# Optimization experiments

Hardware: AMD Instinct MI355X
Metric: run time of the kernel (lower is better)

The kernel has to match this reference:

```python
import jax, jax.numpy as jnp
import numpy as np

LOG2PI = float(np.log(2.0 * np.pi))
NUM_GROUPS = 32
WEIGHTS_THRESHOLD = 0.01
ACTIVATION_THRESHOLD = 1e-9


def _cdist(a, b):
    # a: (..., N, 3), b: (..., M, 3) -> (..., N, M) euclidean distances
    d2 = (jnp.sum(a * a, -1)[..., :, None]
          + jnp.sum(b * b, -1)[..., None, :]
          - 2.0 * jnp.einsum('...nd,...md->...nm', a, b))
    return jnp.sqrt(jnp.maximum(d2, 0.0))


def setup_inputs() -> dict:
    key = jax.random.key(0)
    ks = jax.random.split(key, 7)
    B, V, O, G = 16, 778, 8192, NUM_GROUPS
    verts = jax.random.normal(ks[0], (B, V, 3), jnp.float32)
    anchor_verts = jax.random.normal(ks[1], (B, G, 3), jnp.float32)
    obj_pts = jax.random.normal(ks[2], (B, O, 3), jnp.float32)
    raw = jax.random.normal(ks[3], (B, G, 12), jnp.float32)
    mean = raw[..., :3]
    M = raw[..., 3:].reshape(B, G, 3, 3)
    cov = jnp.einsum('bgij,bgkj->bgik', M, M) + 1e-2 * jnp.eye(3, dtype=jnp.float32)
    contact_gaussians = jnp.concatenate([mean, cov.reshape(B, G, 9)], axis=-1)
    obj_normals = jax.random.normal(ks[4], (B, O, 6), jnp.float32)
    init_verts = jax.random.normal(ks[5], (V, 3), jnp.float32)
    init_anchors = jax.random.normal(ks[6], (G, 3), jnp.float32)
    return dict(verts=verts, anchor_verts=anchor_verts, obj_pts=obj_pts,
                contact_gaussians=contact_gaussians, obj_normals=obj_normals,
                init_verts=init_verts, init_anchors=init_anchors, K=5)


def reference(verts, anchor_verts, obj_pts, contact_gaussians, obj_normals,
              init_verts, init_anchors, K):
    B, V, _ = verts.shape
    G = NUM_GROUPS
    # __init__: assign each vertex to its closest anchor (partition into 32 groups)
    gid = jnp.argmin(_cdist(init_verts, init_anchors), axis=-1)  # (V,)

    # KNN: K smallest distances vertex -> object points
    neigh = _cdist(verts, obj_pts)                 # (B, V, O)
    knn = -jax.lax.top_k(-neigh, K)[0]             # (B, V, K)

    # Per-group MVN log-prob for every vertex (G=32 small, V=778 small)
    mean = contact_gaussians[:, :, :3] + anchor_verts          # (B, G, 3)
    cov = contact_gaussians[:, :, 3:].reshape(B, G, 3, 3)
    L = jnp.linalg.cholesky(cov)                               # (B, G, 3, 3)
    diff = verts[:, None, :, :] - mean[:, :, None, :]          # (B, G, V, 3)
    y = jax.scipy.linalg.solve_triangular(L[:, :, None], diff[..., None], lower=True)[..., 0]
    maha = jnp.sum(y * y, -1)                                  # (B, G, V)
    half_logdet = jnp.sum(jnp.log(jnp.diagonal(L, axis1=-2, axis2=-1)), -1)  # (B, G)
    logp = -0.5 * (maha + 3.0 * LOG2PI) - half_logdet[:, :, None]
    w_all = jnp.exp(logp)                                      # (B, G, V)
    # pick each vertex's own group's weight
    idx = jnp.broadcast_to(gid[None, None, :], (B, 1, V))
    w = jnp.take_along_axis(w_all, idx, axis=1)[:, 0]          # (B, V)

    # per-group min/max normalization (masked, groups partition the vertices)
    grp_mask = gid[None, :] == jnp.arange(G)[:, None]          # (G, V)
    seg_min = jnp.min(jnp.where(grp_mask[None], w[:, None, :], jnp.inf), -1)   # (B, G)
    seg_max = jnp.max(jnp.where(grp_mask[None], w[:, None, :], -jnp.inf), -1)  # (B, G)
    mn = seg_min[:, gid]
    mx = seg_max[:, gid]
    wn = (w - mn) / (mx - mn)
    wn = jnp.where(wn > WEIGHTS_THRESHOLD, wn, 0.0)

    # group activation: torch.allclose(cg[:, i], 0) over whole batch -> zero weight
    active = jnp.any(jnp.abs(contact_gaussians) > ACTIVATION_THRESHOLD, axis=(0, 2))  # (G,)
    eff = jnp.where(active[gid][None, :], wn, 0.0)             # (B, V)
    distances = knn * eff[..., None]
    d_mean = jnp.mean(distances)

    # penetration regularizer using nearest object normal
    ovd = _cdist(verts, obj_normals[..., :3])                  # (B, V, O)
    nn_idx = jnp.argmin(ovd, -1)                               # (B, V)
    nn = jnp.take_along_axis(obj_normals, nn_idx[..., None], axis=1)  # (B, V, 6)
    roots = nn[..., :3] - 0.002 * nn[..., 3:]
    dp = jnp.einsum('bvi,bvi->bv', nn[..., 3:], verts - roots)
    pen = jnp.mean(jax.nn.relu(-dp))
    return (d_mean, pen)
```

## Files before the change

kernel.cpp:

```cpp
#include <hip/hip_runtime.h>
#include <math.h>

#define BB 16
#define VV 778
#define OO 8192
#define GG 32
#define KNN 5
#define VHALF 389
#define THREE_LOG2PI 5.513631199228036f

#define MED3 __builtin_amdgcn_fmed3f

__device__ __forceinline__ void insert5_med3(float (&t)[KNN], float s) {
    t[4] = MED3(s, t[3], t[4]);
    t[3] = MED3(s, t[2], t[3]);
    t[2] = MED3(s, t[1], t[2]);
    t[1] = MED3(s, t[0], t[1]);
    t[0] = fminf(t[0], s);
}

__device__ __forceinline__ void merge5_med3(float (&m)[KNN], const float (&b)[KNN]) {
    m[4] = MED3(b[0], m[3], m[4]);
    m[3] = MED3(b[0], m[2], m[3]);
    m[2] = MED3(b[0], m[1], m[2]);
    m[1] = MED3(b[0], m[0], m[1]);
    m[0] = fminf(m[0], b[0]);
    m[4] = MED3(b[1], m[3], m[4]);
    m[3] = MED3(b[1], m[2], m[3]);
    m[2] = MED3(b[1], m[1], m[2]);
    m[1] = fminf(m[1], b[1]);
    m[4] = MED3(b[2], m[3], m[4]);
    m[3] = MED3(b[2], m[2], m[3]);
    m[2] = fminf(m[2], b[2]);
    m[4] = MED3(b[3], m[3], m[4]);
    m[3] = fminf(m[3], b[3]);
    m[4] = fminf(m[4], b[4]);
}

template <int LOGP1, int LOGP2>
__global__ __launch_bounds__(256) void scan_kernel(
    const float* __restrict__ verts,
    const float* __restrict__ anchor_verts,
    const float* __restrict__ obj_pts,
    const float* __restrict__ contact_gaussians,
    const float* __restrict__ obj_normals,
    const float* __restrict__ init_verts,
    const float* __restrict__ init_anchors,
    int* __restrict__ gid_ws,
    float* __restrict__ active_ws,
    float* __restrict__ segmn,
    float* __restrict__ segmx,
    float* __restrict__ w_ws,
    float* __restrict__ top5,
    float* __restrict__ nns,
    int* __restrict__ nni,
    float* __restrict__ out) {
    constexpr int P1 = 1 << LOGP1;
    constexpr int NPTS1 = OO >> LOGP1;
    constexpr int CH1 = (NPTS1 < 512) ? NPTS1 : 512;
    constexpr int P2 = 1 << LOGP2;
    constexpr int NPTS2 = OO >> LOGP2;
    constexpr int CH2 = (NPTS2 < 512) ? NPTS2 : 512;
    constexpr int CHMAX = (CH1 > CH2) ? CH1 : CH2;

    __shared__ float4 tile[CHMAX];
    __shared__ float anc[GG * 4];
    __shared__ float cholb[GG * 10];
    __shared__ unsigned short gidl[VV];
    __shared__ unsigned int smn[GG], smx[GG];

    int tid = threadIdx.x;
    int bid = blockIdx.x;

    if (bid < BB * 2 * P1) {
        int vc = bid & 1;
        int p = (bid >> 1) & (P1 - 1);
        int b = bid >> (1 + LOGP1);

        int v0 = vc * VHALF + tid;
        bool val1 = (256 + tid) < VHALF;
        int v1 = v0 + (val1 ? 256 : 0);

        float X0, Y0, Z0, X1, Y1, Z1;
        {
            const float* vp = verts + ((size_t)b * VV + v0) * 3;
            X0 = -2.0f * vp[0]; Y0 = -2.0f * vp[1]; Z0 = -2.0f * vp[2];
            const float* vq = verts + ((size_t)b * VV + v1) * 3;
            X1 = -2.0f * vq[0]; Y1 = -2.0f * vq[1]; Z1 = -2.0f * vq[2];
        }

        float t0[KNN], t1[KNN];
#pragma unroll
        for (int k = 0; k < KNN; ++k) { t0[k] = INFINITY; t1[k] = INFINITY; }

        const float* pb = obj_pts + ((size_t)b * OO + p * NPTS1) * 3;
        for (int c0 = 0; c0 < NPTS1; c0 += CH1) {
            for (int j = tid; j < CH1; j += 256) {
                const float* q = pb + (size_t)(c0 + j) * 3;
                float a0 = q[0], a1 = q[1], a2 = q[2];
                tile[j] = make_float4(a0, a1, a2, a0 * a0 + a1 * a1 + a2 * a2);
            }
            __syncthreads();
#pragma unroll 8
            for (int i = 0; i < CH1; ++i) {
                float4 q = tile[i];
                float s0 = fmaf(X0, q.x, fmaf(Y0, q.y, fmaf(Z0, q.z, q.w)));
                float s1 = fmaf(X1, q.x, fmaf(Y1, q.y, fmaf(Z1, q.z, q.w)));
                insert5_med3(t0, s0);
                insert5_med3(t1, s1);
            }
            __syncthreads();
        }
        {
            size_t base = ((size_t)(b * P1 + p) * KNN) * VV;
#pragma unroll
            for (int k = 0; k < KNN; ++k) top5[base + (size_t)k * VV + v0] = t0[k];
            if (val1) {
#pragma unroll
                for (int k = 0; k < KNN; ++k) top5[base + (size_t)k * VV + v1] = t1[k];
            }
        }
        return;
    }

    {
        int sub = bid - BB * 2 * P1;
        int vc = sub & 1;
        int p = (sub >> 1) & (P2 - 1);
        int b = sub >> (1 + LOGP2);

        bool wduty = (p == 0 && vc == 0);
        bool aduty = (p == 0 && vc == 1 && b == 0);
        if (wduty || aduty) {
            if (tid < GG) {
                float x = init_anchors[tid * 3 + 0];
                float y = init_anchors[tid * 3 + 1];
                float z = init_anchors[tid * 3 + 2];
                anc[tid * 4 + 0] = x; anc[tid * 4 + 1] = y;
                anc[tid * 4 + 2] = z; anc[tid * 4 + 3] = x * x + y * y + z * z;
                smn[tid] = 0x7F800000u;
                smx[tid] = 0u;
                if (wduty) {
                    const float* cg2 = contact_gaussians + ((size_t)b * GG + tid) * 12;
                    const float* av = anchor_verts + ((size_t)b * GG + tid) * 3;
                    float c00 = cg2[3];
                    float c10 = cg2[6], c11 = cg2[7];
                    float c20 = cg2[9], c21 = cg2[10], c22 = cg2[11];
                    float L00 = sqrtf(c00);
                    float L10 = c10 / L00;
                    float L20 = c20 / L00;
                    float L11 = sqrtf(c11 - L10 * L10);
                    float L21 = (c21 - L20 * L10) / L11;
                    float L22 = sqrtf(c22 - L20 * L20 - L21 * L21);
                    float* c = cholb + tid * 10;
                    c[0] = L00; c[1] = L10; c[2] = L11;
                    c[3] = L20; c[4] = L21; c[5] = L22;
                    c[6] = logf(L00) + logf(L11) + logf(L22);
                    c[7] = cg2[0] + av[0];
                    c[8] = cg2[1] + av[1];
                    c[9] = cg2[2] + av[2];
                }
            }
            __syncthreads();
            for (int v = tid; v < VV; v += 256) {
                float x = init_verts[v * 3 + 0];
                float y = init_verts[v * 3 + 1];
                float z = init_verts[v * 3 + 2];
                float vv = x * x + y * y + z * z;
                float best = INFINITY;
                int bg = 0;
                for (int g = 0; g < GG; ++g) {
                    float d2 = vv + anc[g * 4 + 3] -
                               2.0f * (x * anc[g * 4 + 0] + y * anc[g * 4 + 1] + z * anc[g * 4 + 2]);
                    d2 = fmaxf(d2, 0.0f);
                    if (d2 < best) { best = d2; bg = g; }
                }
                gidl[v] = (unsigned short)bg;
                if (aduty) gid_ws[v] = bg;
            }
            __syncthreads();
            if (wduty) {
                for (int v = tid; v < VV; v += 256) {
                    int g = gidl[v];
                    const float* c = cholb + g * 10;
                    const float* vp = verts + ((size_t)b * VV + v) * 3;
                    float d0 = vp[0] - c[7];
                    float d1 = vp[1] - c[8];
                    float d2 = vp[2] - c[9];
                    float y0 = d0 / c[0];
                    float y1 = (d1 - c[1] * y0) / c[2];
                    float y2 = (d2 - c[3] * y0 - c[4] * y1) / c[5];
                    float maha = y0 * y0 + y1 * y1 + y2 * y2;
                    float wv = expf(-0.5f * (maha + THREE_LOG2PI) - c[6]);
                    w_ws[(size_t)b * VV + v] = wv;
                    unsigned int u = __float_as_uint(wv);
                    atomicMin(&smn[g], u);
                    atomicMax(&smx[g], u);
                }
                __syncthreads();
                if (tid < GG) {
                    segmn[b * GG + tid] = __uint_as_float(smn[tid]);
                    segmx[b * GG + tid] = __uint_as_float(smx[tid]);
                }
            }
            if (aduty) {
                if (tid < GG) {
                    int any = 0;
                    for (int bb = 0; bb < BB && !any; ++bb) {
                        for (int c = 0; c < 12; ++c) {
                            if (fabsf(contact_gaussians[((size_t)bb * GG + tid) * 12 + c]) > 1e-9f) {
                                any = 1;
                                break;
                            }
                        }
                    }
                    active_ws[tid] = any ? 1.0f : 0.0f;
                }
                if (tid == 0) { out[0] = 0.0f; out[1] = 0.0f; }
            }
            __syncthreads();
        }

        int v0 = vc * VHALF + tid;
        bool val1 = (256 + tid) < VHALF;
        int v1 = v0 + (val1 ? 256 : 0);

        float X0, Y0, Z0, X1, Y1, Z1;
        {
            const float* vp = verts + ((size_t)b * VV + v0) * 3;
            X0 = -2.0f * vp[0]; Y0 = -2.0f * vp[1]; Z0 = -2.0f * vp[2];
            const float* vq = verts + ((size_t)b * VV + v1) * 3;
            X1 = -2.0f * vq[0]; Y1 = -2.0f * vq[1]; Z1 = -2.0f * vq[2];
        }

        float bs0 = INFINITY, bs1 = INFINITY;
        int bi0 = 0, bi1 = 0;
        const float* nbp = obj_normals + ((size_t)b * OO + p * NPTS2) * 6;
        for (int c0 = 0; c0 < NPTS2; c0 += CH2) {
            for (int j = tid; j < CH2; j += 256) {
                const float* r = nbp + (size_t)(c0 + j) * 6;
                float b0 = r[0], b1 = r[1], b2 = r[2];
                tile[j] = make_float4(b0, b1, b2, b0 * b0 + b1 * b1 + b2 * b2);
            }
            __syncthreads();
#pragma unroll 8
            for (int i = 0; i < CH2; ++i) {
                float4 n = tile[i];
                float u0 = fmaf(X0, n.x, fmaf(Y0, n.y, fmaf(Z0, n.z, n.w)));
                float u1 = fmaf(X1, n.x, fmaf(Y1, n.y, fmaf(Z1, n.z, n.w)));
                int gi = c0 + i;
                if (u0 < bs0) { bs0 = u0; bi0 = gi; }
                if (u1 < bs1) { bs1 = u1; bi1 = gi; }
            }
            __syncthreads();
        }
        {
            size_t o = (size_t)(b * P2 + p) * VV + v0;
            nns[o] = bs0;
            nni[o] = p * NPTS2 + bi0;
            if (val1) {
                size_t o1 = (size_t)(b * P2 + p) * VV + v1;
                nns[o1] = bs1;
                nni[o1] = p * NPTS2 + bi1;
            }
        }
    }
}

template <int LOGP1, int LOGP2>
__global__ __launch_bounds__(256) void finalize_kernel(
    const float* __restrict__ top5,
    const float* __restrict__ nns,
    const int* __restrict__ nni,
    const float* __restrict__ obj_normals,
    const float* __restrict__ verts,
    const int* __restrict__ gid,
    const float* __restrict__ w,
    const float* __restrict__ segmn,
    const float* __restrict__ segmx,
    const float* __restrict__ active,
    float* __restrict__ out) {
    constexpr int P1 = 1 << LOGP1;
    constexpr int P2 = 1 << LOGP2;
    constexpr int NM1 = (P1 + 3) / 4;
    constexpr int NM2 = (P2 + 3) / 4;
    constexpr int NCH = (VV + 63) / 64;

    __shared__ float mt[4][KNN][64];
    __shared__ float sb[4][64];
    __shared__ int ib[4][64];
    __shared__ float rd[256], rp[256];

    int tid = threadIdx.x;
    int pi = tid >> 6;
    int vi = tid & 63;
    int b = blockIdx.x / NCH;
    int chunk = blockIdx.x - b * NCH;
    int v = chunk * 64 + vi;
    bool valid = v < VV;

    float m[KNN];
#pragma unroll
    for (int k = 0; k < KNN; ++k) m[k] = INFINITY;
    if (valid) {
#pragma unroll
        for (int r = 0; r < NM1; ++r) {
            int p = pi * NM1 + r;
            if (p < P1) {
                size_t base = ((size_t)(b * P1 + p) * KNN) * VV + v;
                float t[KNN];
#pragma unroll
                for (int k = 0; k < KNN; ++k) t[k] = top5[base + (size_t)k * VV];
                merge5_med3(m, t);
            }
        }
    }

    float bs = INFINITY;
    int bi = 0x7FFFFFFF;
    if (valid) {
#pragma unroll
        for (int r = 0; r < NM2; ++r) {
            int p = pi * NM2 + r;
            if (p < P2) {
                size_t o = (size_t)(b * P2 + p) * VV + v;
                float s = nns[o];
                int i = nni[o];
                if (s < bs || (s == bs && i < bi)) { bs = s; bi = i; }
            }
        }
    }

#pragma unroll
    for (int k = 0; k < KNN; ++k) mt[pi][k][vi] = m[k];
    sb[pi][vi] = bs;
    ib[pi][vi] = bi;
    __syncthreads();

    if (pi < 2) {
        float t[KNN];
#pragma unroll
        for (int k = 0; k < KNN; ++k) t[k] = mt[pi + 2][k][vi];
        merge5_med3(m, t);
#pragma unroll
        for (int k = 0; k < KNN; ++k) mt[pi][k][vi] = m[k];
        float s = sb[pi + 2][vi];
        int i = ib[pi + 2][vi];
        if (s < bs || (s == bs && i < bi)) { bs = s; bi = i; }
        sb[pi][vi] = bs;
        ib[pi][vi] = bi;
    }
    __syncthreads();

    float cd = 0.0f, cp = 0.0f;
    if (pi == 0 && valid) {
        float t[KNN];
#pragma unroll
        for (int k = 0; k < KNN; ++k) t[k] = mt[1][k][vi];
        merge5_med3(m, t);
        float s = sb[1][vi];
        int i = ib[1][vi];
        if (s < bs || (s == bs && i < bi)) { bs = s; bi = i; }

        const float* vp = verts + ((size_t)b * VV + v) * 3;
        float vx = vp[0], vy = vp[1], vz = vp[2];
        float vv = vx * vx + vy * vy + vz * vz;

        int g = gid[v];
        float wv = w[(size_t)b * VV + v];
        float mn = segmn[b * GG + g];
        float mx = segmx[b * GG + g];
        float wn = (wv - mn) / (mx - mn);
        float eff = (active[g] != 0.0f && wn > 0.01f) ? wn : 0.0f;
        float sk = 0.0f;
#pragma unroll
        for (int k = 0; k < KNN; ++k) sk += sqrtf(fmaxf(vv + m[k], 0.0f));
        cd = eff * sk;

        const float* row = obj_normals + ((size_t)b * OO + bi) * 6;
        float n0 = row[3], n1 = row[4], n2 = row[5];
        float r0 = row[0] - 0.002f * n0;
        float r1 = row[1] - 0.002f * n1;
        float r2 = row[2] - 0.002f * n2;
        float dp = n0 * (vx - r0) + n1 * (vy - r1) + n2 * (vz - r2);
        cp = fmaxf(-dp, 0.0f);
    }

    rd[tid] = cd;
    rp[tid] = cp;
    __syncthreads();
    for (int s = 128; s > 0; s >>= 1) {
        if (tid < s) {
            rd[tid] += rd[tid + s];
            rp[tid] += rp[tid + s];
        }
        __syncthreads();
    }
    if (tid == 0) {
        atomicAdd(&out[0], rd[0] * (1.0f / ((float)BB * VV * KNN)));
        atomicAdd(&out[1], rp[0] * (1.0f / ((float)BB * VV)));
    }
}

template <int LOGP1, int LOGP2>
static void launch_all(const float* verts, const float* anchor_verts,
                       const float* obj_pts, const float* contact_gaussians,
                       const float* obj_normals, const float* init_verts,
                       const float* init_anchors, int* gid_ws, float* active_ws,
                       float* segmn, float* segmx, float* w_ws, float* top5,
                       float* nns, int* nni, float* out, hipStream_t stream) {
    constexpr int P1 = 1 << LOGP1;
    constexpr int P2 = 1 << LOGP2;
    constexpr int NCH = (VV + 63) / 64;
    dim3 block(256);
    hipLaunchKernelGGL((scan_kernel<LOGP1, LOGP2>), dim3(BB * 2 * (P1 + P2)), block,
                       0, stream, verts, anchor_verts, obj_pts, contact_gaussians,
                       obj_normals, init_verts, init_anchors, gid_ws, active_ws,
                       segmn, segmx, w_ws, top5, nns, nni, out);
    hipLaunchKernelGGL((finalize_kernel<LOGP1, LOGP2>), dim3(BB * NCH),
                       block, 0, stream, top5, nns, nni, obj_normals, verts,
                       gid_ws, w_ws, segmn, segmx, active_ws, out);
}

extern "C" void kernel_launch(void* const* d_in, const int* in_sizes, int n_in,
                              void* d_out, int out_size, void* d_ws, size_t ws_size,
                              hipStream_t stream) {
    const float* verts = (const float*)d_in[0];
    const float* anchor_verts = (const float*)d_in[1];
    const float* obj_pts = (const float*)d_in[2];
    const float* contact_gaussians = (const float*)d_in[3];
    const float* obj_normals = (const float*)d_in[4];
    const float* init_verts = (const float*)d_in[5];
    const float* init_anchors = (const float*)d_in[6];
    float* out = (float*)d_out;

    char* ws = (char*)d_ws;
    int* gid_ws = (int*)(ws + 0);
    float* active_ws = (float*)(ws + 4096);
    float* segmn = (float*)(ws + 4224);
    float* segmx = (float*)(ws + 6272);
    float* w_ws = (float*)(ws + 8320);
    const size_t base = 58112;

    int logP1 = 5;
    while (logP1 > 0) {
        int P1 = 1 << logP1, P2 = 1 << (logP1 > 0 ? logP1 - 1 : 0);
        if (base + (size_t)BB * VV * 4 * (P1 * KNN + P2 * 2) <= ws_size) break;
        --logP1;
    }
    int P1 = 1 << logP1;
    int logP2 = logP1 > 0 ? logP1 - 1 : 0;
    int P2 = 1 << logP2;

    float* top5 = (float*)(ws + base);
    float* nns = (float*)(ws + base + (size_t)BB * P1 * KNN * VV * 4);
    int* nni = (int*)(ws + base + (size_t)BB * VV * 4 * (P1 * KNN + P2));

#define LAUNCH(L1, L2)                                                         \
    launch_all<L1, L2>(verts, anchor_verts, obj_pts, contact_gaussians,        \
                       obj_normals, init_verts, init_anchors, gid_ws,          \
                       active_ws, segmn, segmx, w_ws, top5, nns, nni, out,     \
                       stream)
    switch (logP1) {
        case 5: LAUNCH(5, 4); break;
        case 4: LAUNCH(4, 3); break;
        case 3: LAUNCH(3, 2); break;
        case 2: LAUNCH(2, 1); break;
        case 1: LAUNCH(1, 0); break;
        default: LAUNCH(0, 0); break;
    }
#undef LAUNCH
}
```

Baseline: 144.1 us.

## Process all vertices per block and reduce nearest-normal index with 64-bit atomicMin

Each scan block now covers all 778 vertices (four per thread) instead of splitting them across two blocks, so every loaded object tile is reused across twice as many vertices. The nearest-normal partial results are no longer written to workspace and merged in finalize. Instead each block packs an order-preserving distance key and the point index into a 64-bit value and applies atomicMin, which needs a memset before launch. The nearest-normal search gets as many partitions as the KNN scan. The price is higher register pressure, fewer and larger blocks, and an extra memset launch.

```diff
diff --git a/kernel.cpp b/kernel.cpp
--- a/kernel.cpp
+++ b/kernel.cpp
@@ -6,7 +6,6 @@
 #define OO 8192
 #define GG 32
 #define KNN 5
-#define VHALF 389
 #define THREE_LOG2PI 5.513631199228036f
 
 #define MED3 __builtin_amdgcn_fmed3f
@@ -37,6 +36,12 @@
     m[4] = fminf(m[4], b[4]);
 }
 
+__device__ __forceinline__ unsigned int fkey(float s) {
+    unsigned int u = __float_as_uint(s);
+    unsigned int m = (u & 0x80000000u) ? 0xFFFFFFFFu : 0x80000000u;
+    return u ^ m;
+}
+
 template <int LOGP1, int LOGP2>
 __global__ __launch_bounds__(256) void scan_kernel(
     const float* __restrict__ verts,
@@ -52,8 +57,7 @@
     float* __restrict__ segmx,
     float* __restrict__ w_ws,
     float* __restrict__ top5,
-    float* __restrict__ nns,
-    int* __restrict__ nni,
+    unsigned long long* __restrict__ amin,
     float* __restrict__ out) {
     constexpr int P1 = 1 << LOGP1;
     constexpr int NPTS1 = OO >> LOGP1;
@@ -72,26 +76,26 @@
     int tid = threadIdx.x;
     int bid = blockIdx.x;
 
-    if (bid < BB * 2 * P1) {
-        int vc = bid & 1;
-        int p = (bid >> 1) & (P1 - 1);
-        int b = bid >> (1 + LOGP1);
-
-        int v0 = vc * VHALF + tid;
-        bool val1 = (256 + tid) < VHALF;
-        int v1 = v0 + (val1 ? 256 : 0);
-
-        float X0, Y0, Z0, X1, Y1, Z1;
-        {
-            const float* vp = verts + ((size_t)b * VV + v0) * 3;
-            X0 = -2.0f * vp[0]; Y0 = -2.0f * vp[1]; Z0 = -2.0f * vp[2];
-            const float* vq = verts + ((size_t)b * VV + v1) * 3;
-            X1 = -2.0f * vq[0]; Y1 = -2.0f * vq[1]; Z1 = -2.0f * vq[2];
-        }
-
-        float t0[KNN], t1[KNN];
-#pragma unroll
-        for (int k = 0; k < KNN; ++k) { t0[k] = INFINITY; t1[k] = INFINITY; }
+    if (bid < BB * P1) {
+        int p = bid & (P1 - 1);
+        int b = bid >> LOGP1;
+
+        float X[4], Y[4], Z[4];
+#pragma unroll
+        for (int s = 0; s < 4; ++s) {
+            int v = tid + s * 256;
+            if (v >= VV) v = VV - 1;
+            const float* vp = verts + ((size_t)b * VV + v) * 3;
+            X[s] = -2.0f * vp[0];
+            Y[s] = -2.0f * vp[1];
+            Z[s] = -2.0f * vp[2];
+        }
+
+        float t[4][KNN];
+#pragma unroll
+        for (int s = 0; s < 4; ++s)
+#pragma unroll
+            for (int k = 0; k < KNN; ++k) t[s][k] = INFINITY;
 
         const float* pb = obj_pts + ((size_t)b * OO + p * NPTS1) * 3;
         for (int c0 = 0; c0 < NPTS1; c0 += CH1) {
@@ -101,36 +105,39 @@
                 tile[j] = make_float4(a0, a1, a2, a0 * a0 + a1 * a1 + a2 * a2);
             }
             __syncthreads();
-#pragma unroll 8
+#pragma unroll 4
             for (int i = 0; i < CH1; ++i) {
                 float4 q = tile[i];
-                float s0 = fmaf(X0, q.x, fmaf(Y0, q.y, fmaf(Z0, q.z, q.w)));
-                float s1 = fmaf(X1, q.x, fmaf(Y1, q.y, fmaf(Z1, q.z, q.w)));
-                insert5_med3(t0, s0);
-                insert5_med3(t1, s1);
+#pragma unroll
+                for (int s = 0; s < 4; ++s) {
+                    float sv = fmaf(X[s], q.x, fmaf(Y[s], q.y, fmaf(Z[s], q.z, q.w)));
+                    insert5_med3(t[s], sv);
+                }
             }
             __syncthreads();
         }
         {
             size_t base = ((size_t)(b * P1 + p) * KNN) * VV;
 #pragma unroll
-            for (int k = 0; k < KNN; ++k) top5[base + (size_t)k * VV + v0] = t0[k];
-            if (val1) {
-#pragma unroll
-                for (int k = 0; k < KNN; ++k) top5[base + (size_t)k * VV + v1] = t1[k];
+            for (int s = 0; s < 4; ++s) {
+                int v = tid + s * 256;
+                if (v < VV) {
+#pragma unroll
+                    for (int k = 0; k < KNN; ++k)
+                        top5[base + (size_t)k * VV + v] = t[s][k];
+                }
             }
         }
         return;
     }
 
     {
-        int sub = bid - BB * 2 * P1;
-        int vc = sub & 1;
-        int p = (sub >> 1) & (P2 - 1);
-        int b = sub >> (1 + LOGP2);
-
-        bool wduty = (p == 0 && vc == 0);
-        bool aduty = (p == 0 && vc == 1 && b == 0);
+        int sub = bid - BB * P1;
+        int p = sub & (P2 - 1);
+        int b = sub >> LOGP2;
+
+        bool wduty = (p == 0);
+        bool aduty = (p == 1 && b == 0);
         if (wduty || aduty) {
             if (tid < GG) {
                 float x = init_anchors[tid * 3 + 0];
@@ -221,20 +228,22 @@
             __syncthreads();
         }
 
-        int v0 = vc * VHALF + tid;
-        bool val1 = (256 + tid) < VHALF;
-        int v1 = v0 + (val1 ? 256 : 0);
-
-        float X0, Y0, Z0, X1, Y1, Z1;
-        {
-            const float* vp = verts + ((size_t)b * VV + v0) * 3;
-            X0 = -2.0f * vp[0]; Y0 = -2.0f * vp[1]; Z0 = -2.0f * vp[2];
-            const float* vq = verts + ((size_t)b * VV + v1) * 3;
-            X1 = -2.0f * vq[0]; Y1 = -2.0f * vq[1]; Z1 = -2.0f * vq[2];
-        }
-
-        float bs0 = INFINITY, bs1 = INFINITY;
-        int bi0 = 0, bi1 = 0;
+        float X[4], Y[4], Z[4];
+#pragma unroll
+        for (int s = 0; s < 4; ++s) {
+            int v = tid + s * 256;
+            if (v >= VV) v = VV - 1;
+            const float* vp = verts + ((size_t)b * VV + v) * 3;
+            X[s] = -2.0f * vp[0];
+            Y[s] = -2.0f * vp[1];
+            Z[s] = -2.0f * vp[2];
+        }
+
+        float bs[4];
+        int bi[4];
+#pragma unroll
+        for (int s = 0; s < 4; ++s) { bs[s] = INFINITY; bi[s] = 0; }
+
         const float* nbp = obj_normals + ((size_t)b * OO + p * NPTS2) * 6;
         for (int c0 = 0; c0 < NPTS2; c0 += CH2) {
             for (int j = tid; j < CH2; j += 256) {
@@ -243,35 +252,35 @@
                 tile[j] = make_float4(b0, b1, b2, b0 * b0 + b1 * b1 + b2 * b2);
             }
             __syncthreads();
-#pragma unroll 8
+#pragma unroll 4
             for (int i = 0; i < CH2; ++i) {
                 float4 n = tile[i];
-                float u0 = fmaf(X0, n.x, fmaf(Y0, n.y, fmaf(Z0, n.z, n.w)));
-                float u1 = fmaf(X1, n.x, fmaf(Y1, n.y, fmaf(Z1, n.z, n.w)));
                 int gi = c0 + i;
-                if (u0 < bs0) { bs0 = u0; bi0 = gi; }
-                if (u1 < bs1) { bs1 = u1; bi1 = gi; }
-            }
-            __syncthreads();
-        }
-        {
-            size_t o = (size_t)(b * P2 + p) * VV + v0;
-            nns[o] = bs0;
-            nni[o] = p * NPTS2 + bi0;
-            if (val1) {
-                size_t o1 = (size_t)(b * P2 + p) * VV + v1;
-                nns[o1] = bs1;
-                nni[o1] = p * NPTS2 + bi1;
-            }
-        }
-    }
-}
-
-template <int LOGP1, int LOGP2>
+#pragma unroll
+                for (int s = 0; s < 4; ++s) {
+                    float u = fmaf(X[s], n.x, fmaf(Y[s], n.y, fmaf(Z[s], n.z, n.w)));
+                    if (u < bs[s]) { bs[s] = u; bi[s] = gi; }
+                }
+            }
+            __syncthreads();
+        }
+#pragma unroll
+        for (int s = 0; s < 4; ++s) {
+            int v = tid + s * 256;
+            if (v < VV) {
+                unsigned long long key =
+                    ((unsigned long long)fkey(bs[s]) << 32) |
+                    (unsigned int)(p * NPTS2 + bi[s]);
+                atomicMin(&amin[(size_t)b * VV + v], key);
+            }
+        }
+    }
+}
+
+template <int LOGP1>
 __global__ __launch_bounds__(256) void finalize_kernel(
     const float* __restrict__ top5,
-    const float* __restrict__ nns,
-    const int* __restrict__ nni,
+    const unsigned long long* __restrict__ amin,
     const float* __restrict__ obj_normals,
     const float* __restrict__ verts,
     const int* __restrict__ gid,
@@ -281,14 +290,10 @@
     const float* __restrict__ active,
     float* __restrict__ out) {
     constexpr int P1 = 1 << LOGP1;
-    constexpr int P2 = 1 << LOGP2;
     constexpr int NM1 = (P1 + 3) / 4;
-    constexpr int NM2 = (P2 + 3) / 4;
     constexpr int NCH = (VV + 63) / 64;
 
     __shared__ float mt[4][KNN][64];
-    __shared__ float sb[4][64];
-    __shared__ int ib[4][64];
     __shared__ float rd[256], rp[256];
 
     int tid = threadIdx.x;
@@ -316,25 +321,8 @@
         }
     }
 
-    float bs = INFINITY;
-    int bi = 0x7FFFFFFF;
-    if (valid) {
-#pragma unroll
-        for (int r = 0; r < NM2; ++r) {
-            int p = pi * NM2 + r;
-            if (p < P2) {
-                size_t o = (size_t)(b * P2 + p) * VV + v;
-                float s = nns[o];
-                int i = nni[o];
-                if (s < bs || (s == bs && i < bi)) { bs = s; bi = i; }
-            }
-        }
-    }
-
 #pragma unroll
     for (int k = 0; k < KNN; ++k) mt[pi][k][vi] = m[k];
-    sb[pi][vi] = bs;
-    ib[pi][vi] = bi;
     __syncthreads();
 
     if (pi < 2) {
@@ -344,11 +332,6 @@
         merge5_med3(m, t);
 #pragma unroll
         for (int k = 0; k < KNN; ++k) mt[pi][k][vi] = m[k];
-        float s = sb[pi + 2][vi];
-        int i = ib[pi + 2][vi];
-        if (s < bs || (s == bs && i < bi)) { bs = s; bi = i; }
-        sb[pi][vi] = bs;
-        ib[pi][vi] = bi;
     }
     __syncthreads();
 
@@ -358,9 +341,6 @@
 #pragma unroll
         for (int k = 0; k < KNN; ++k) t[k] = mt[1][k][vi];
         merge5_med3(m, t);
-        float s = sb[1][vi];
-        int i = ib[1][vi];
-        if (s < bs || (s == bs && i < bi)) { bs = s; bi = i; }
 
         const float* vp = verts + ((size_t)b * VV + v) * 3;
         float vx = vp[0], vy = vp[1], vz = vp[2];
@@ -377,6 +357,7 @@
         for (int k = 0; k < KNN; ++k) sk += sqrtf(fmaxf(vv + m[k], 0.0f));
         cd = eff * sk;
 
+        int bi = (int)(unsigned int)(amin[(size_t)b * VV + v] & 0xFFFFFFFFull);
         const float* row = obj_normals + ((size_t)b * OO + bi) * 6;
         float n0 = row[3], n1 = row[4], n2 = row[5];
         float r0 = row[0] - 0.002f * n0;
@@ -402,24 +383,23 @@
     }
 }
 
-template <int LOGP1, int LOGP2>
+template <int LOGP>
 static void launch_all(const float* verts, const float* anchor_verts,
                        const float* obj_pts, const float* contact_gaussians,
                        const float* obj_normals, const float* init_verts,
                        const float* init_anchors, int* gid_ws, float* active_ws,
                        float* segmn, float* segmx, float* w_ws, float* top5,
-                       float* nns, int* nni, float* out, hipStream_t stream) {
-    constexpr int P1 = 1 << LOGP1;
-    constexpr int P2 = 1 << LOGP2;
+                       unsigned long long* amin, float* out, hipStream_t stream) {
+    constexpr int P = 1 << LOGP;
     constexpr int NCH = (VV + 63) / 64;
     dim3 block(256);
-    hipLaunchKernelGGL((scan_kernel<LOGP1, LOGP2>), dim3(BB * 2 * (P1 + P2)), block,
+    hipLaunchKernelGGL((scan_kernel<LOGP, LOGP>), dim3(BB * 2 * P), block,
                        0, stream, verts, anchor_verts, obj_pts, contact_gaussians,
                        obj_normals, init_verts, init_anchors, gid_ws, active_ws,
-                       segmn, segmx, w_ws, top5, nns, nni, out);
-    hipLaunchKernelGGL((finalize_kernel<LOGP1, LOGP2>), dim3(BB * NCH),
-                       block, 0, stream, top5, nns, nni, obj_normals, verts,
-                       gid_ws, w_ws, segmn, segmx, active_ws, out);
+                       segmn, segmx, w_ws, top5, amin, out);
+    hipLaunchKernelGGL((finalize_kernel<LOGP>), dim3(BB * NCH), block, 0, stream,
+                       top5, amin, obj_normals, verts, gid_ws, w_ws, segmn,
+                       segmx, active_ws, out);
 }
 
 extern "C" void kernel_launch(void* const* d_in, const int* in_sizes, int n_in,
@@ -440,34 +420,30 @@
     float* segmn = (float*)(ws + 4224);
     float* segmx = (float*)(ws + 6272);
     float* w_ws = (float*)(ws + 8320);
-    const size_t base = 58112;
-
-    int logP1 = 5;
-    while (logP1 > 0) {
-        int P1 = 1 << logP1, P2 = 1 << (logP1 > 0 ? logP1 - 1 : 0);
-        if (base + (size_t)BB * VV * 4 * (P1 * KNN + P2 * 2) <= ws_size) break;
-        --logP1;
-    }
-    int P1 = 1 << logP1;
-    int logP2 = logP1 > 0 ? logP1 - 1 : 0;
-    int P2 = 1 << logP2;
+    unsigned long long* amin = (unsigned long long*)(ws + 58112);
+    const size_t base = 157696;
+
+    int logP = 5;
+    while (logP > 0 &&
+           base + (size_t)BB * (1 << logP) * KNN * VV * 4 > ws_size)
+        --logP;
 
     float* top5 = (float*)(ws + base);
-    float* nns = (float*)(ws + base + (size_t)BB * P1 * KNN * VV * 4);
-    int* nni = (int*)(ws + base + (size_t)BB * VV * 4 * (P1 * KNN + P2));
-
-#define LAUNCH(L1, L2)                                                         \
-    launch_all<L1, L2>(verts, anchor_verts, obj_pts, contact_gaussians,        \
-                       obj_normals, init_verts, init_anchors, gid_ws,          \
-                       active_ws, segmn, segmx, w_ws, top5, nns, nni, out,     \
-                       stream)
-    switch (logP1) {
-        case 5: LAUNCH(5, 4); break;
-        case 4: LAUNCH(4, 3); break;
-        case 3: LAUNCH(3, 2); break;
-        case 2: LAUNCH(2, 1); break;
-        case 1: LAUNCH(1, 0); break;
-        default: LAUNCH(0, 0); break;
+
+    hipMemsetAsync(amin, 0xFF, (size_t)BB * VV * sizeof(unsigned long long),
+                   stream);
+
+#define LAUNCH(L)                                                              \
+    launch_all<L>(verts, anchor_verts, obj_pts, contact_gaussians,             \
+                  obj_normals, init_verts, init_anchors, gid_ws, active_ws,    \
+                  segmn, segmx, w_ws, top5, amin, out, stream)
+    switch (logP) {
+        case 5: LAUNCH(5); break;
+        case 4: LAUNCH(4); break;
+        case 3: LAUNCH(3); break;
+        case 2: LAUNCH(2); break;
+        case 1: LAUNCH(1); break;
+        default: LAUNCH(0); break;
     }
 #undef LAUNCH
 }
```

New measurement: 140.4 us. -2.6%, faster.
